# Kernel tuning notes

Measured on AMD Instinct MI355X. Metric: run time of the kernel, lower is better.

Reference implementation:

```python
import jax, jax.numpy as jnp
import numpy as np

DIM = 1024
T = 16384
WINDOW = 32
DIM_HEAD = 64
HEADS = DIM // DIM_HEAD  # 16
EPS = 1e-5


def setup_inputs() -> dict:
    key = jax.random.key(0)
    k1, k2, k3 = jax.random.split(key, 3)
    x = jax.random.normal(k1, (DIM, T), dtype=jnp.float32)
    w_qkv = jax.random.normal(k2, (3 * DIM, DIM), dtype=jnp.float32) / np.float32(np.sqrt(DIM))
    w_out = jax.random.normal(k3, (DIM, DIM), dtype=jnp.float32) / np.float32(np.sqrt(DIM))
    gamma = jnp.ones((DIM,), dtype=jnp.float32)
    beta = jnp.zeros((DIM,), dtype=jnp.float32)
    return {"x": x, "w_qkv": w_qkv, "w_out": w_out, "gamma": gamma, "beta": beta}


def _rotate_half(t):
    # original: split channels into (2, d/2), swap halves with negation
    d = t.shape[-1]
    return jnp.concatenate((-t[..., d // 2:], t[..., :d // 2]), axis=-1)


def reference(x, w_qkv, w_out, gamma, beta):
    C, Tn = x.shape
    xt = x.T  # (T, C)
    # LayerNorm over channel dim (eqx.nn.LayerNorm, eps=1e-5)
    mu = jnp.mean(xt, axis=-1, keepdims=True)
    var = jnp.var(xt, axis=-1, keepdims=True)
    normed = (xt - mu) * jax.lax.rsqrt(var + EPS) * gamma + beta
    # QKV projection (Linear with weight (out,in), no bias)
    qkv = normed @ w_qkv.T  # (T, 3C)
    q, k, v = jnp.split(qkv, 3, axis=-1)
    w = Tn // WINDOW
    def towin(t):  # (w n) (h d) -> h w n d
        return t.reshape(w, WINDOW, HEADS, DIM_HEAD).transpose(2, 0, 1, 3)
    q, k, v = map(towin, (q, k, v))
    # rotary pos emb over window positions (use_xpos=False -> scale == 1)
    inv_freq = 1.0 / (10000.0 ** (jnp.arange(0, DIM_HEAD, 2, dtype=jnp.float32) / DIM_HEAD))
    tpos = jnp.arange(WINDOW, dtype=jnp.float32)
    freqs = jnp.einsum('i,j->ij', tpos, inv_freq)  # (n, d/2)
    freqs = jnp.concatenate((freqs, freqs), axis=-1)  # (n, d)
    cos, sin = jnp.cos(freqs), jnp.sin(freqs)
    q = q * cos + _rotate_half(q) * sin
    k = k * cos + _rotate_half(k) * sin
    # per-head, per-window full (non-causal) attention
    scale = DIM_HEAD ** -0.5
    logits = jnp.einsum('hwnd,hwmd->hwnm', q, k) * scale
    attn = jax.nn.softmax(logits, axis=-1)
    out = jnp.einsum('hwnm,hwmd->hwnd', attn, v)
    out = out.transpose(1, 2, 0, 3).reshape(Tn, C)  # h w n d -> (w n) (h d)
    out = out @ w_out.T
    return out.T + x
```

## Files before the change

### kernel.cpp

```cpp
#include <hip/hip_runtime.h>

#define T_TOK 16384
#define C_DIM 1024

typedef float f32x4 __attribute__((ext_vector_type(4)));
typedef float f32x16 __attribute__((ext_vector_type(16)));
typedef __bf16 bf16x8 __attribute__((ext_vector_type(8)));
typedef unsigned short u16x8 __attribute__((ext_vector_type(8)));
typedef unsigned short u16x4 __attribute__((ext_vector_type(4)));

__device__ __forceinline__ unsigned short f2bf(float f) {
  union { float f; unsigned u; } v; v.f = f;
  unsigned r = v.u + 0x7fffu + ((v.u >> 16) & 1u);
  return (unsigned short)(r >> 16);
}
__device__ __forceinline__ float bf2f(unsigned short h) {
  union { unsigned u; float f; } v; v.u = ((unsigned)h) << 16;
  return v.f;
}
__device__ __forceinline__ unsigned pk2(float a, float b) {
  return (unsigned)f2bf(a) | ((unsigned)f2bf(b) << 16);
}

__global__ __launch_bounds__(256) void cvt_kernel(const float* __restrict__ in,
                                                  unsigned short* __restrict__ out, int n4) {
  int i = blockIdx.x * 256 + threadIdx.x;
  if (i >= n4) return;
  f32x4 v = *(const f32x4*)(in + (size_t)i * 4);
  u16x4 o;
#pragma unroll
  for (int j = 0; j < 4; ++j) o[j] = f2bf(v[j]);
  *(u16x4*)(out + (size_t)i * 4) = o;
}

__global__ __launch_bounds__(256) void rope_tab_kernel(float* __restrict__ tab) {
  int idx = blockIdx.x * 256 + threadIdx.x;
  if (idx >= 1024) return;
  int mm = idx >> 5, d = idx & 31;
  float invf = powf(10000.f, -(float)d * (1.f / 32.f));
  float ang = (float)mm * invf;
  float s, c;
  sincosf(ang, &s, &c);
  tab[idx * 2] = c;
  tab[idx * 2 + 1] = s;
}

__global__ __launch_bounds__(256) void ln_stats_kernel(const float* __restrict__ x,
                                                       float* __restrict__ mu,
                                                       float* __restrict__ rstd) {
  __shared__ float s1[4][64];
  __shared__ float s2[4][64];
  const int tid = threadIdx.x;
  const int lt = tid & 63, cq = tid >> 6;
  const int t = blockIdx.x * 64 + lt;
  float s = 0.f, ss = 0.f;
  const float* p = x + (size_t)cq * 256 * T_TOK + t;
  for (int c = 0; c < 256; ++c) {
    float v = p[(size_t)c * T_TOK];
    s += v; ss += v * v;
  }
  s1[cq][lt] = s; s2[cq][lt] = ss;
  __syncthreads();
  if (tid < 64) {
    float S  = s1[0][tid] + s1[1][tid] + s1[2][tid] + s1[3][tid];
    float SS = s2[0][tid] + s2[1][tid] + s2[2][tid] + s2[3][tid];
    float m = S * (1.f / 1024.f);
    float var = SS * (1.f / 1024.f) - m * m;
    mu[blockIdx.x * 64 + tid] = m;
    rstd[blockIdx.x * 64 + tid] = rsqrtf(var + 1e-5f);
  }
}

__global__ __launch_bounds__(256) void ln_tr_kernel(const float* __restrict__ x,
                                                    const float* __restrict__ mu,
                                                    const float* __restrict__ rstd,
                                                    const float* __restrict__ gamma,
                                                    const float* __restrict__ beta,
                                                    unsigned short* __restrict__ normed) {
  __shared__ float tile[64][65];
  __shared__ float gs[64], bs[64], ms[64], rs[64];
  const int tid = threadIdx.x;
  const int bt = blockIdx.x & 255;
  const int bc = blockIdx.x >> 8;
  const int t0 = bt * 64, c0 = bc * 64;
  if (tid < 64) {
    gs[tid] = gamma[c0 + tid];
    bs[tid] = beta[c0 + tid];
    ms[tid] = mu[t0 + tid];
    rs[tid] = rstd[t0 + tid];
  }
  const int lc = tid >> 4;
  const int lt4 = (tid & 15) * 4;
#pragma unroll
  for (int r = 0; r < 4; ++r) {
    int c = r * 16 + lc;
    f32x4 v = *(const f32x4*)&x[(size_t)(c0 + c) * T_TOK + t0 + lt4];
    tile[c][lt4 + 0] = v[0]; tile[c][lt4 + 1] = v[1];
    tile[c][lt4 + 2] = v[2]; tile[c][lt4 + 3] = v[3];
  }
  __syncthreads();
#pragma unroll
  for (int r = 0; r < 2; ++r) {
    int idx = r * 256 + tid;
    int t = idx >> 3;
    int c8 = (idx & 7) * 8;
    float m = ms[t], rr = rs[t];
    u16x8 o;
#pragma unroll
    for (int j = 0; j < 8; ++j) {
      float v = tile[c8 + j][t];
      v = (v - m) * rr * gs[c8 + j] + bs[c8 + j];
      o[j] = f2bf(v);
    }
    *(u16x8*)&normed[(size_t)(t0 + t) * C_DIM + c0 + c8] = o;
  }
}

#define GLDS(gp, lp) \
  __builtin_amdgcn_global_load_lds((const __attribute__((address_space(1))) void*)(gp), \
                                   (__attribute__((address_space(3))) void*)(lp), 16, 0, 0)

#define BARF() do { __builtin_amdgcn_s_barrier(); asm volatile("" ::: "memory"); } while (0)
#define VMC(n) asm volatile("s_waitcnt vmcnt(" #n ")" ::: "memory")

template <int EPI>
__global__ __launch_bounds__(512, 2) void gemm8p_kernel(const unsigned short* __restrict__ A,
                                                        const unsigned short* __restrict__ B,
                                                        unsigned short* __restrict__ Obf,
                                                        int ldo, int nbn, int K,
                                                        const float* __restrict__ Xadd,
                                                        float* __restrict__ Ofp) {
  __shared__ unsigned short Lds[2][2][2][8192];
  const int tid = threadIdx.x;
  const int w = tid >> 6, lane = tid & 63;
  const int wm = w >> 2, wn = w & 3;

  const int nbm = gridDim.x / nbn;
  const int xcd = blockIdx.x & 7;
  const int ib = blockIdx.x >> 3;
  int mt, nt;
  if ((nbm & 7) == 0) {
    const int mtpx = nbm >> 3;
    mt = xcd * mtpx + (ib % mtpx);
    nt = ib / mtpx;
  } else {
    const int ntpx = nbn >> 3;
    nt = xcd * ntpx + (ib % ntpx);
    mt = ib / ntpx;
  }
  const size_t m0 = (size_t)mt * 256, n0 = (size_t)nt * 256;

  const unsigned short* gA = A + (m0 + (lane >> 3)) * (size_t)K + ((lane & 7) ^ (lane >> 3)) * 8;
  const unsigned short* gB = B + (n0 + (lane >> 3)) * (size_t)K + ((lane & 7) ^ (lane >> 3)) * 8;
  const int wrow = w * 8;

  auto stageA = [&](int b, int h, int kt) {
    const unsigned short* g = gA + (size_t)(h * 128) * K + (size_t)kt * 64;
    GLDS(g + (size_t)wrow * K,        &Lds[0][b][h][wrow * 64]);
    GLDS(g + (size_t)(64 + wrow) * K, &Lds[0][b][h][(64 + wrow) * 64]);
  };
  auto stageB = [&](int b, int h, int kt) {
    const unsigned short* g = gB + (size_t)(h * 128) * K + (size_t)kt * 64;
    GLDS(g + (size_t)wrow * K,        &Lds[1][b][h][wrow * 64]);
    GLDS(g + (size_t)(64 + wrow) * K, &Lds[1][b][h][(64 + wrow) * 64]);
  };

  f32x4 acc[8][4];
#pragma unroll
  for (int i = 0; i < 8; ++i)
#pragma unroll
    for (int j = 0; j < 4; ++j) acc[i][j] = (f32x4){0.f, 0.f, 0.f, 0.f};

  const int KT = K >> 6;
  const int off_r = (lane & 15) * 64;
  const int slot0 = (((lane >> 4) ^ (lane & 7)) * 8);
  const int slot1 = slot0 ^ 32;
  const int boff = (wn & 1) * 4096;

  bf16x8 aLo[4][2], aHi[4][2], bLo[2][2], bHi[2][2];

  stageA(0, 0, 0); stageA(0, 1, 0); stageB(0, 0, 0); stageB(0, 1, 0);
  if (KT > 1) {
    stageB(1, 0, 1); stageB(1, 1, 1); stageA(1, 0, 1); stageA(1, 1, 1);
    VMC(8);
  } else {
    VMC(0);
  }
  BARF();

  int bb = 0;
  for (int t = 0; t < KT; ++t, bb ^= 1) {
    const unsigned short* Ab = &Lds[0][bb][wm][0];
    const unsigned short* Bb = &Lds[1][bb][wn >> 1][boff];

#pragma unroll
    for (int mi = 0; mi < 4; ++mi) {
      aLo[mi][0] = *(const bf16x8*)&Ab[mi * 1024 + off_r + slot0];
      aLo[mi][1] = *(const bf16x8*)&Ab[mi * 1024 + off_r + slot1];
    }
#pragma unroll
    for (int ni = 0; ni < 2; ++ni) {
      bLo[ni][0] = *(const bf16x8*)&Bb[ni * 1024 + off_r + slot0];
      bLo[ni][1] = *(const bf16x8*)&Bb[ni * 1024 + off_r + slot1];
      bHi[ni][0] = *(const bf16x8*)&Bb[(ni + 2) * 1024 + off_r + slot0];
      bHi[ni][1] = *(const bf16x8*)&Bb[(ni + 2) * 1024 + off_r + slot1];
    }

    __builtin_amdgcn_s_setprio(1);
#pragma unroll
    for (int mi = 0; mi < 4; ++mi)
#pragma unroll
      for (int ni = 0; ni < 2; ++ni)
#pragma unroll
        for (int ks = 0; ks < 2; ++ks)
          acc[mi][ni] = __builtin_amdgcn_mfma_f32_16x16x32_bf16(aLo[mi][ks], bLo[ni][ks], acc[mi][ni], 0, 0, 0);
    __builtin_amdgcn_s_setprio(0);

#pragma unroll
    for (int mi = 0; mi < 4; ++mi) {
      aHi[mi][0] = *(const bf16x8*)&Ab[(mi + 4) * 1024 + off_r + slot0];
      aHi[mi][1] = *(const bf16x8*)&Ab[(mi + 4) * 1024 + off_r + slot1];
    }

    __builtin_amdgcn_s_setprio(1);
#pragma unroll
    for (int mi = 0; mi < 4; ++mi)
#pragma unroll
      for (int ni = 0; ni < 2; ++ni)
#pragma unroll
        for (int ks = 0; ks < 2; ++ks)
          acc[mi][ni + 2] = __builtin_amdgcn_mfma_f32_16x16x32_bf16(aLo[mi][ks], bHi[ni][ks], acc[mi][ni + 2], 0, 0, 0);
    __builtin_amdgcn_s_setprio(0);
    BARF();

    if (t + 2 < KT) { stageB(bb, 0, t + 2); stageB(bb, 1, t + 2); }

    __builtin_amdgcn_s_setprio(1);
#pragma unroll
    for (int mi = 0; mi < 4; ++mi)
#pragma unroll
      for (int ni = 0; ni < 2; ++ni)
#pragma unroll
        for (int ks = 0; ks < 2; ++ks)
          acc[mi + 4][ni + 2] = __builtin_amdgcn_mfma_f32_16x16x32_bf16(aHi[mi][ks], bHi[ni][ks], acc[mi + 4][ni + 2], 0, 0, 0);
    __builtin_amdgcn_s_setprio(0);
    BARF();

    if (t + 2 < KT) { stageA(bb, 0, t + 2); stageA(bb, 1, t + 2); }

    __builtin_amdgcn_s_setprio(1);
#pragma unroll
    for (int mi = 0; mi < 4; ++mi)
#pragma unroll
      for (int ni = 0; ni < 2; ++ni)
#pragma unroll
        for (int ks = 0; ks < 2; ++ks)
          acc[mi + 4][ni] = __builtin_amdgcn_mfma_f32_16x16x32_bf16(aHi[mi][ks], bLo[ni][ks], acc[mi + 4][ni], 0, 0, 0);
    __builtin_amdgcn_s_setprio(0);

    if (t + 2 < KT) {
      VMC(8);
    } else {
      VMC(0);
    }
    BARF();
  }

  if (EPI == 0) {
    unsigned short* cw = &Lds[0][0][0][0] + (size_t)w * 8192;
#pragma unroll
    for (int mi = 0; mi < 8; ++mi)
#pragma unroll
      for (int ni = 0; ni < 4; ++ni)
#pragma unroll
        for (int r = 0; r < 4; ++r)
          cw[(mi * 16 + (lane >> 4) * 4 + r) * 64 + ni * 16 + (lane & 15)] = f2bf(acc[mi][ni][r]);
    const size_t gr0 = m0 + wm * 128;
    const size_t gc0 = n0 + wn * 64;
#pragma unroll
    for (int it = 0; it < 16; ++it) {
      int idx = it * 64 + lane;
      int rr = idx >> 3, c8 = (idx & 7) * 8;
      *(u16x8*)&Obf[(gr0 + rr) * (size_t)ldo + gc0 + c8] = *(const u16x8*)&cw[rr * 64 + c8];
    }
  } else {
    const size_t mrow0 = m0 + wm * 128 + (lane >> 4) * 4;
    const size_t ncol0 = n0 + wn * 64 + (lane & 15);
#pragma unroll
    for (int mi = 0; mi < 8; ++mi)
#pragma unroll
      for (int ni = 0; ni < 4; ++ni)
#pragma unroll
        for (int r = 0; r < 4; ++r) {
          size_t o = (mrow0 + mi * 16 + r) * T_TOK + ncol0 + ni * 16;
          Ofp[o] = acc[mi][ni][r] + Xadd[o];
        }
  }
}

__global__ __launch_bounds__(256) void attn_kernel(const unsigned short* __restrict__ qkv,
                                                   const float* __restrict__ ropeT,
                                                   unsigned short* __restrict__ aout) {
  __shared__ unsigned short Vt[4][64][32];
  const int tid = threadIdx.x;
  const int wv = tid >> 6;
  const int lane = tid & 63;
  const int m = lane & 31;
  const int hi = lane >> 5;
  const int gw = blockIdx.x * 4 + wv;
  const int w = gw >> 4, h = gw & 15;
  const size_t rowbase = ((size_t)(w * 32 + m)) * 3072 + (size_t)h * 64;
  const unsigned short* qp = qkv + rowbase;

  u16x8 qv[4], kv[4], vv[4];
#pragma unroll
  for (int s = 0; s < 4; ++s) {
    int off = s * 16 + hi * 8;
    qv[s] = *(const u16x8*)(qp + off);
    kv[s] = *(const u16x8*)(qp + 1024 + off);
    vv[s] = *(const u16x8*)(qp + 2048 + off);
  }

#pragma unroll
  for (int s = 0; s < 4; ++s)
#pragma unroll
    for (int j = 0; j < 8; ++j) {
      int d = s * 16 + hi * 8 + j;
      int slot = (((m >> 3) ^ (d ^ (d >> 2))) & 3) * 8 + (m & 7);
      Vt[wv][d][slot] = vv[s][j];
    }

  f32x4 ct[2][4];
  const float* tp = ropeT + (size_t)(m * 32 + hi * 8) * 2;
#pragma unroll
  for (int kp = 0; kp < 2; ++kp)
#pragma unroll
    for (int q = 0; q < 4; ++q)
      ct[kp][q] = *(const f32x4*)(tp + kp * 32 + q * 4);

  union FU { unsigned u[4]; bf16x8 v; };
  bf16x8 qfr[4], kfr[4];
#pragma unroll
  for (int ks = 0; ks < 4; ++ks) {
    const int kp = ks & 1;
    FU fq, fk;
#pragma unroll
    for (int jp = 0; jp < 4; ++jp) {
      float c0 = ct[kp][jp][0], s0 = ct[kp][jp][1];
      float c1 = ct[kp][jp][2], s1 = ct[kp][jp][3];
      float q0 = bf2f(qv[ks][2 * jp]), q1 = bf2f(qv[ks][2 * jp + 1]);
      float k0 = bf2f(kv[ks][2 * jp]), k1 = bf2f(kv[ks][2 * jp + 1]);
      float rq0, rq1, rk0, rk1;
      if (ks < 2) {
        rq0 = -bf2f(qv[ks + 2][2 * jp]); rq1 = -bf2f(qv[ks + 2][2 * jp + 1]);
        rk0 = -bf2f(kv[ks + 2][2 * jp]); rk1 = -bf2f(kv[ks + 2][2 * jp + 1]);
      } else {
        rq0 = bf2f(qv[ks - 2][2 * jp]); rq1 = bf2f(qv[ks - 2][2 * jp + 1]);
        rk0 = bf2f(kv[ks - 2][2 * jp]); rk1 = bf2f(kv[ks - 2][2 * jp + 1]);
      }
      fq.u[jp] = pk2(q0 * c0 + rq0 * s0, q1 * c1 + rq1 * s1);
      fk.u[jp] = pk2(k0 * c0 + rk0 * s0, k1 * c1 + rk1 * s1);
    }
    qfr[ks] = fq.v; kfr[ks] = fk.v;
  }

  f32x16 accS;
#pragma unroll
  for (int i = 0; i < 16; ++i) accS[i] = 0.f;
#pragma unroll
  for (int ks = 0; ks < 4; ++ks)
    accS = __builtin_amdgcn_mfma_f32_32x32x16_bf16(kfr[ks], qfr[ks], accS, 0, 0, 0);

  float p[16];
  float mx = -1e30f;
#pragma unroll
  for (int r = 0; r < 16; ++r) { p[r] = accS[r] * 0.125f; mx = fmaxf(mx, p[r]); }
  mx = fmaxf(mx, __shfl_xor(mx, 32, 64));
  float sum = 0.f;
#pragma unroll
  for (int r = 0; r < 16; ++r) { p[r] = __expf(p[r] - mx); sum += p[r]; }
  sum += __shfl_xor(sum, 32, 64);
  const float inv = 1.f / sum;
#pragma unroll
  for (int r = 0; r < 16; ++r) p[r] *= inv;

  bf16x8 pfr[2];
  {
    FU f0, f1;
    unsigned a0 = hi ? pk2(p[0], p[1]) : pk2(p[4], p[5]);
    unsigned a1 = hi ? pk2(p[2], p[3]) : pk2(p[6], p[7]);
    unsigned b0 = (unsigned)__shfl_xor((int)a0, 32, 64);
    unsigned b1 = (unsigned)__shfl_xor((int)a1, 32, 64);
    if (hi) { f0.u[0] = b0; f0.u[1] = b1; f0.u[2] = pk2(p[4], p[5]); f0.u[3] = pk2(p[6], p[7]); }
    else    { f0.u[0] = pk2(p[0], p[1]); f0.u[1] = pk2(p[2], p[3]); f0.u[2] = b0; f0.u[3] = b1; }
    unsigned a2 = hi ? pk2(p[8], p[9])   : pk2(p[12], p[13]);
    unsigned a3 = hi ? pk2(p[10], p[11]) : pk2(p[14], p[15]);
    unsigned b2 = (unsigned)__shfl_xor((int)a2, 32, 64);
    unsigned b3 = (unsigned)__shfl_xor((int)a3, 32, 64);
    if (hi) { f1.u[0] = b2; f1.u[1] = b3; f1.u[2] = pk2(p[12], p[13]); f1.u[3] = pk2(p[14], p[15]); }
    else    { f1.u[0] = pk2(p[8], p[9]); f1.u[1] = pk2(p[10], p[11]); f1.u[2] = b2; f1.u[3] = b3; }
    pfr[0] = f0.v; pfr[1] = f1.v;
  }

  f32x16 accO[2];
#pragma unroll
  for (int i = 0; i < 16; ++i) { accO[0][i] = 0.f; accO[1][i] = 0.f; }
  const int dl = lane & 31;
#pragma unroll
  for (int dh = 0; dh < 2; ++dh) {
    int d = dh * 32 + dl;
    int sx = (d ^ (d >> 2)) & 3;
#pragma unroll
    for (int ks = 0; ks < 2; ++ks) {
      bf16x8 vf = *(const bf16x8*)&Vt[wv][d][(((2 * ks + hi) ^ sx) & 3) * 8];
      accO[dh] = __builtin_amdgcn_mfma_f32_32x32x16_bf16(pfr[ks], vf, accO[dh], 0, 0, 0);
    }
  }

#pragma unroll
  for (int r = 0; r < 16; ++r) {
    int n = (r & 3) + 8 * (r >> 2) + 4 * hi;
    size_t o = (size_t)(w * 32 + n) * 1024 + h * 64 + dl;
    aout[o] = f2bf(accO[0][r]);
    aout[o + 32] = f2bf(accO[1][r]);
  }
}

extern "C" void kernel_launch(void* const* d_in, const int* in_sizes, int n_in,
                              void* d_out, int out_size, void* d_ws, size_t ws_size,
                              hipStream_t stream) {
  const float* x     = (const float*)d_in[0];
  const float* w_qkv = (const float*)d_in[1];
  const float* w_out = (const float*)d_in[2];
  const float* gamma = (const float*)d_in[3];
  const float* beta  = (const float*)d_in[4];

  char* ws = (char*)d_ws;
  unsigned short* wqkv_bf = (unsigned short*)(ws);
  unsigned short* wout_bf = (unsigned short*)(ws + 6291456);
  float* mu    = (float*)(ws + 8388608);
  float* rstd  = (float*)(ws + 8454144);
  float* ropeT = (float*)(ws + 8519680);
  unsigned short* normed = (unsigned short*)(ws + 8527872);
  unsigned short* qkv    = (unsigned short*)(ws + 42082304);
  unsigned short* aout   = normed;

  cvt_kernel<<<3072, 256, 0, stream>>>(w_qkv, wqkv_bf, 3072 * 1024 / 4);
  cvt_kernel<<<1024, 256, 0, stream>>>(w_out, wout_bf, 1024 * 1024 / 4);
  rope_tab_kernel<<<4, 256, 0, stream>>>(ropeT);
  ln_stats_kernel<<<256, 256, 0, stream>>>(x, mu, rstd);
  ln_tr_kernel<<<4096, 256, 0, stream>>>(x, mu, rstd, gamma, beta, normed);
  gemm8p_kernel<0><<<768, 512, 0, stream>>>(normed, wqkv_bf, qkv, 3072, 12, 1024,
                                            nullptr, nullptr);
  attn_kernel<<<2048, 256, 0, stream>>>(qkv, ropeT, aout);
  gemm8p_kernel<1><<<256, 512, 0, stream>>>(wout_bf, aout, nullptr, 0, 64, 1024,
                                            x, (float*)d_out);
}
```

Baseline: 211.3 us.

## Fuse QKV projection GEMM with windowed attention in one kernel

After: 205.8 us. 2.6% less time.

```diff
diff --git a/kernel.cpp b/kernel.cpp
--- a/kernel.cpp
+++ b/kernel.cpp
@@ -123,6 +123,226 @@
 #define BARF() do { __builtin_amdgcn_s_barrier(); asm volatile("" ::: "memory"); } while (0)
 #define VMC(n) asm volatile("s_waitcnt vmcnt(" #n ")" ::: "memory")
 
+__global__ __launch_bounds__(512, 2) void qkvattn_kernel(const unsigned short* __restrict__ A,
+                                                         const unsigned short* __restrict__ Bq,
+                                                         const float* __restrict__ ropeT,
+                                                         unsigned short* __restrict__ aout) {
+  __shared__ unsigned short arena[57344];
+  unsigned short* LA = arena;
+  unsigned short* LB = arena + 32768;
+  unsigned short* QKl = arena;
+  unsigned short* Vtl = arena + 34816;
+
+  const int tid = threadIdx.x;
+  const int w = tid >> 6, lane = tid & 63;
+  const int wm = w >> 1, wn = w & 1;
+  const int K = 1024, KT = 16;
+
+  const int xcd = blockIdx.x & 7;
+  const int ib = blockIdx.x >> 3;
+  const int tt = xcd * 8 + (ib & 7);
+  const int h = ib >> 3;
+  const size_t m0 = (size_t)tt * 256;
+
+  const int preslot = ((lane & 7) ^ (lane >> 3)) * 8;
+  const unsigned short* gA = A + (m0 + w * 8 + (lane >> 3)) * (size_t)K + preslot;
+  const unsigned short* gB0 = Bq + ((size_t)(0 + h * 64 + w * 8 + (lane >> 3))) * K + preslot;
+  const unsigned short* gB1 = Bq + ((size_t)(1024 + h * 64 + w * 8 + (lane >> 3))) * K + preslot;
+  const unsigned short* gB2 = Bq + ((size_t)(2048 + h * 64 + w * 8 + (lane >> 3))) * K + preslot;
+
+  auto stage7 = [&](int b, int kt) {
+    const size_t k0 = (size_t)kt * 64;
+    GLDS(gA + k0,                      LA + b * 16384 + (w * 8) * 64);
+    GLDS(gA + (size_t)64 * K + k0,     LA + b * 16384 + (64 + w * 8) * 64);
+    GLDS(gA + (size_t)128 * K + k0,    LA + b * 16384 + (128 + w * 8) * 64);
+    GLDS(gA + (size_t)192 * K + k0,    LA + b * 16384 + (192 + w * 8) * 64);
+    GLDS(gB0 + k0,                     LB + b * 12288 + (w * 8) * 64);
+    GLDS(gB1 + k0,                     LB + b * 12288 + (64 + w * 8) * 64);
+    GLDS(gB2 + k0,                     LB + b * 12288 + (128 + w * 8) * 64);
+  };
+
+  f32x4 acc[4][6];
+#pragma unroll
+  for (int i = 0; i < 4; ++i)
+#pragma unroll
+    for (int j = 0; j < 6; ++j) acc[i][j] = (f32x4){0.f, 0.f, 0.f, 0.f};
+
+  const int off_r = (lane & 15) * 64;
+  const int slot0 = (((lane >> 4) ^ (lane & 7)) * 8);
+  const int slot1 = slot0 ^ 32;
+
+  stage7(0, 0);
+  stage7(1, 1);
+  VMC(7);
+  BARF();
+
+  int bb = 0;
+  for (int t = 0; t < KT; ++t, bb ^= 1) {
+    const unsigned short* Ab = LA + bb * 16384 + (wm * 64) * 64;
+    const unsigned short* Bb = LB + bb * 12288 + (wn * 96) * 64;
+
+    bf16x8 aF[4][2], bF[6][2];
+#pragma unroll
+    for (int mi = 0; mi < 4; ++mi) {
+      aF[mi][0] = *(const bf16x8*)&Ab[mi * 1024 + off_r + slot0];
+      aF[mi][1] = *(const bf16x8*)&Ab[mi * 1024 + off_r + slot1];
+    }
+#pragma unroll
+    for (int ni = 0; ni < 6; ++ni) {
+      bF[ni][0] = *(const bf16x8*)&Bb[ni * 1024 + off_r + slot0];
+      bF[ni][1] = *(const bf16x8*)&Bb[ni * 1024 + off_r + slot1];
+    }
+
+    __builtin_amdgcn_s_setprio(1);
+#pragma unroll
+    for (int mi = 0; mi < 4; ++mi)
+#pragma unroll
+      for (int ni = 0; ni < 6; ++ni)
+#pragma unroll
+        for (int ks = 0; ks < 2; ++ks)
+          acc[mi][ni] = __builtin_amdgcn_mfma_f32_16x16x32_bf16(aF[mi][ks], bF[ni][ks], acc[mi][ni], 0, 0, 0);
+    __builtin_amdgcn_s_setprio(0);
+    BARF();
+
+    if (t + 2 < KT) {
+      stage7(bb, t + 2);
+      VMC(7);
+    } else {
+      VMC(0);
+    }
+    BARF();
+  }
+
+  __syncthreads();
+#pragma unroll
+  for (int mi = 0; mi < 4; ++mi)
+#pragma unroll
+    for (int ni = 0; ni < 6; ++ni) {
+      const int j = wn * 96 + ni * 16 + (lane & 15);
+#pragma unroll
+      for (int r = 0; r < 4; ++r) {
+        int tok = wm * 64 + mi * 16 + (lane >> 4) * 4 + r;
+        unsigned short bv = f2bf(acc[mi][ni][r]);
+        if (wn == 0 || ni < 2) {
+          QKl[tok * 136 + j] = bv;
+        } else {
+          int d = j - 128;
+          int mm = tok & 31, win = tok >> 5;
+          Vtl[(win * 64 + d) * 32 + ((((mm >> 3) ^ (d ^ (d >> 2))) & 3) * 8 + (mm & 7))] = bv;
+        }
+      }
+    }
+  __syncthreads();
+
+  {
+    const int m = lane & 31, hi = lane >> 5;
+    const unsigned short* qp = QKl + (size_t)(w * 32 + m) * 136;
+    u16x8 qv[4], kv[4];
+#pragma unroll
+    for (int s = 0; s < 4; ++s) {
+      int off = s * 16 + hi * 8;
+      qv[s] = *(const u16x8*)(qp + off);
+      kv[s] = *(const u16x8*)(qp + 64 + off);
+    }
+
+    f32x4 ct[2][4];
+    const float* tp = ropeT + (size_t)(m * 32 + hi * 8) * 2;
+#pragma unroll
+    for (int kp = 0; kp < 2; ++kp)
+#pragma unroll
+      for (int q = 0; q < 4; ++q)
+        ct[kp][q] = *(const f32x4*)(tp + kp * 32 + q * 4);
+
+    union FU { unsigned u[4]; bf16x8 v; };
+    bf16x8 qfr[4], kfr[4];
+#pragma unroll
+    for (int ks = 0; ks < 4; ++ks) {
+      const int kp = ks & 1;
+      FU fq, fk;
+#pragma unroll
+      for (int jp = 0; jp < 4; ++jp) {
+        float c0 = ct[kp][jp][0], s0 = ct[kp][jp][1];
+        float c1 = ct[kp][jp][2], s1 = ct[kp][jp][3];
+        float q0 = bf2f(qv[ks][2 * jp]), q1 = bf2f(qv[ks][2 * jp + 1]);
+        float k0 = bf2f(kv[ks][2 * jp]), k1 = bf2f(kv[ks][2 * jp + 1]);
+        float rq0, rq1, rk0, rk1;
+        if (ks < 2) {
+          rq0 = -bf2f(qv[ks + 2][2 * jp]); rq1 = -bf2f(qv[ks + 2][2 * jp + 1]);
+          rk0 = -bf2f(kv[ks + 2][2 * jp]); rk1 = -bf2f(kv[ks + 2][2 * jp + 1]);
+        } else {
+          rq0 = bf2f(qv[ks - 2][2 * jp]); rq1 = bf2f(qv[ks - 2][2 * jp + 1]);
+          rk0 = bf2f(kv[ks - 2][2 * jp]); rk1 = bf2f(kv[ks - 2][2 * jp + 1]);
+        }
+        fq.u[jp] = pk2(q0 * c0 + rq0 * s0, q1 * c1 + rq1 * s1);
+        fk.u[jp] = pk2(k0 * c0 + rk0 * s0, k1 * c1 + rk1 * s1);
+      }
+      qfr[ks] = fq.v; kfr[ks] = fk.v;
+    }
+
+    f32x16 accS;
+#pragma unroll
+    for (int i = 0; i < 16; ++i) accS[i] = 0.f;
+#pragma unroll
+    for (int ks = 0; ks < 4; ++ks)
+      accS = __builtin_amdgcn_mfma_f32_32x32x16_bf16(kfr[ks], qfr[ks], accS, 0, 0, 0);
+
+    float p[16];
+    float mx = -1e30f;
+#pragma unroll
+    for (int r = 0; r < 16; ++r) { p[r] = accS[r] * 0.125f; mx = fmaxf(mx, p[r]); }
+    mx = fmaxf(mx, __shfl_xor(mx, 32, 64));
+    float sum = 0.f;
+#pragma unroll
+    for (int r = 0; r < 16; ++r) { p[r] = __expf(p[r] - mx); sum += p[r]; }
+    sum += __shfl_xor(sum, 32, 64);
+    const float inv = 1.f / sum;
+#pragma unroll
+    for (int r = 0; r < 16; ++r) p[r] *= inv;
+
+    bf16x8 pfr[2];
+    {
+      FU f0, f1;
+      unsigned a0 = hi ? pk2(p[0], p[1]) : pk2(p[4], p[5]);
+      unsigned a1 = hi ? pk2(p[2], p[3]) : pk2(p[6], p[7]);
+      unsigned b0 = (unsigned)__shfl_xor((int)a0, 32, 64);
+      unsigned b1 = (unsigned)__shfl_xor((int)a1, 32, 64);
+      if (hi) { f0.u[0] = b0; f0.u[1] = b1; f0.u[2] = pk2(p[4], p[5]); f0.u[3] = pk2(p[6], p[7]); }
+      else    { f0.u[0] = pk2(p[0], p[1]); f0.u[1] = pk2(p[2], p[3]); f0.u[2] = b0; f0.u[3] = b1; }
+      unsigned a2 = hi ? pk2(p[8], p[9])   : pk2(p[12], p[13]);
+      unsigned a3 = hi ? pk2(p[10], p[11]) : pk2(p[14], p[15]);
+      unsigned b2 = (unsigned)__shfl_xor((int)a2, 32, 64);
+      unsigned b3 = (unsigned)__shfl_xor((int)a3, 32, 64);
+      if (hi) { f1.u[0] = b2; f1.u[1] = b3; f1.u[2] = pk2(p[12], p[13]); f1.u[3] = pk2(p[14], p[15]); }
+      else    { f1.u[0] = pk2(p[8], p[9]); f1.u[1] = pk2(p[10], p[11]); f1.u[2] = b2; f1.u[3] = b3; }
+      pfr[0] = f0.v; pfr[1] = f1.v;
+    }
+
+    f32x16 accO[2];
+#pragma unroll
+    for (int i = 0; i < 16; ++i) { accO[0][i] = 0.f; accO[1][i] = 0.f; }
+    const int dl = lane & 31;
+#pragma unroll
+    for (int dh = 0; dh < 2; ++dh) {
+      int d = dh * 32 + dl;
+      int sx = (d ^ (d >> 2)) & 3;
+#pragma unroll
+      for (int ks = 0; ks < 2; ++ks) {
+        bf16x8 vf = *(const bf16x8*)&Vtl[(w * 64 + d) * 32 + (((2 * ks + hi) ^ sx) & 3) * 8];
+        accO[dh] = __builtin_amdgcn_mfma_f32_32x32x16_bf16(pfr[ks], vf, accO[dh], 0, 0, 0);
+      }
+    }
+
+    const int W = tt * 8 + w;
+#pragma unroll
+    for (int r = 0; r < 16; ++r) {
+      int n = (r & 3) + 8 * (r >> 2) + 4 * hi;
+      size_t o = (size_t)(W * 32 + n) * 1024 + h * 64 + dl;
+      aout[o] = f2bf(accO[0][r]);
+      aout[o + 32] = f2bf(accO[1][r]);
+    }
+  }
+}
+
 template <int EPI>
 __global__ __launch_bounds__(512, 2) void gemm8p_kernel(const unsigned short* __restrict__ A,
                                                         const unsigned short* __restrict__ B,
@@ -298,134 +518,6 @@
   }
 }
 
-__global__ __launch_bounds__(256) void attn_kernel(const unsigned short* __restrict__ qkv,
-                                                   const float* __restrict__ ropeT,
-                                                   unsigned short* __restrict__ aout) {
-  __shared__ unsigned short Vt[4][64][32];
-  const int tid = threadIdx.x;
-  const int wv = tid >> 6;
-  const int lane = tid & 63;
-  const int m = lane & 31;
-  const int hi = lane >> 5;
-  const int gw = blockIdx.x * 4 + wv;
-  const int w = gw >> 4, h = gw & 15;
-  const size_t rowbase = ((size_t)(w * 32 + m)) * 3072 + (size_t)h * 64;
-  const unsigned short* qp = qkv + rowbase;
-
-  u16x8 qv[4], kv[4], vv[4];
-#pragma unroll
-  for (int s = 0; s < 4; ++s) {
-    int off = s * 16 + hi * 8;
-    qv[s] = *(const u16x8*)(qp + off);
-    kv[s] = *(const u16x8*)(qp + 1024 + off);
-    vv[s] = *(const u16x8*)(qp + 2048 + off);
-  }
-
-#pragma unroll
-  for (int s = 0; s < 4; ++s)
-#pragma unroll
-    for (int j = 0; j < 8; ++j) {
-      int d = s * 16 + hi * 8 + j;
-      int slot = (((m >> 3) ^ (d ^ (d >> 2))) & 3) * 8 + (m & 7);
-      Vt[wv][d][slot] = vv[s][j];
-    }
-
-  f32x4 ct[2][4];
-  const float* tp = ropeT + (size_t)(m * 32 + hi * 8) * 2;
-#pragma unroll
-  for (int kp = 0; kp < 2; ++kp)
-#pragma unroll
-    for (int q = 0; q < 4; ++q)
-      ct[kp][q] = *(const f32x4*)(tp + kp * 32 + q * 4);
-
-  union FU { unsigned u[4]; bf16x8 v; };
-  bf16x8 qfr[4], kfr[4];
-#pragma unroll
-  for (int ks = 0; ks < 4; ++ks) {
-    const int kp = ks & 1;
-    FU fq, fk;
-#pragma unroll
-    for (int jp = 0; jp < 4; ++jp) {
-      float c0 = ct[kp][jp][0], s0 = ct[kp][jp][1];
-      float c1 = ct[kp][jp][2], s1 = ct[kp][jp][3];
-      float q0 = bf2f(qv[ks][2 * jp]), q1 = bf2f(qv[ks][2 * jp + 1]);
-      float k0 = bf2f(kv[ks][2 * jp]), k1 = bf2f(kv[ks][2 * jp + 1]);
-      float rq0, rq1, rk0, rk1;
-      if (ks < 2) {
-        rq0 = -bf2f(qv[ks + 2][2 * jp]); rq1 = -bf2f(qv[ks + 2][2 * jp + 1]);
-        rk0 = -bf2f(kv[ks + 2][2 * jp]); rk1 = -bf2f(kv[ks + 2][2 * jp + 1]);
-      } else {
-        rq0 = bf2f(qv[ks - 2][2 * jp]); rq1 = bf2f(qv[ks - 2][2 * jp + 1]);
-        rk0 = bf2f(kv[ks - 2][2 * jp]); rk1 = bf2f(kv[ks - 2][2 * jp + 1]);
-      }
-      fq.u[jp] = pk2(q0 * c0 + rq0 * s0, q1 * c1 + rq1 * s1);
-      fk.u[jp] = pk2(k0 * c0 + rk0 * s0, k1 * c1 + rk1 * s1);
-    }
-    qfr[ks] = fq.v; kfr[ks] = fk.v;
-  }
-
-  f32x16 accS;
-#pragma unroll
-  for (int i = 0; i < 16; ++i) accS[i] = 0.f;
-#pragma unroll
-  for (int ks = 0; ks < 4; ++ks)
-    accS = __builtin_amdgcn_mfma_f32_32x32x16_bf16(kfr[ks], qfr[ks], accS, 0, 0, 0);
-
-  float p[16];
-  float mx = -1e30f;
-#pragma unroll
-  for (int r = 0; r < 16; ++r) { p[r] = accS[r] * 0.125f; mx = fmaxf(mx, p[r]); }
-  mx = fmaxf(mx, __shfl_xor(mx, 32, 64));
-  float sum = 0.f;
-#pragma unroll
-  for (int r = 0; r < 16; ++r) { p[r] = __expf(p[r] - mx); sum += p[r]; }
-  sum += __shfl_xor(sum, 32, 64);
-  const float inv = 1.f / sum;
-#pragma unroll
-  for (int r = 0; r < 16; ++r) p[r] *= inv;
-
-  bf16x8 pfr[2];
-  {
-    FU f0, f1;
-    unsigned a0 = hi ? pk2(p[0], p[1]) : pk2(p[4], p[5]);
-    unsigned a1 = hi ? pk2(p[2], p[3]) : pk2(p[6], p[7]);
-    unsigned b0 = (unsigned)__shfl_xor((int)a0, 32, 64);
-    unsigned b1 = (unsigned)__shfl_xor((int)a1, 32, 64);
-    if (hi) { f0.u[0] = b0; f0.u[1] = b1; f0.u[2] = pk2(p[4], p[5]); f0.u[3] = pk2(p[6], p[7]); }
-    else    { f0.u[0] = pk2(p[0], p[1]); f0.u[1] = pk2(p[2], p[3]); f0.u[2] = b0; f0.u[3] = b1; }
-    unsigned a2 = hi ? pk2(p[8], p[9])   : pk2(p[12], p[13]);
-    unsigned a3 = hi ? pk2(p[10], p[11]) : pk2(p[14], p[15]);
-    unsigned b2 = (unsigned)__shfl_xor((int)a2, 32, 64);
-    unsigned b3 = (unsigned)__shfl_xor((int)a3, 32, 64);
-    if (hi) { f1.u[0] = b2; f1.u[1] = b3; f1.u[2] = pk2(p[12], p[13]); f1.u[3] = pk2(p[14], p[15]); }
-    else    { f1.u[0] = pk2(p[8], p[9]); f1.u[1] = pk2(p[10], p[11]); f1.u[2] = b2; f1.u[3] = b3; }
-    pfr[0] = f0.v; pfr[1] = f1.v;
-  }
-
-  f32x16 accO[2];
-#pragma unroll
-  for (int i = 0; i < 16; ++i) { accO[0][i] = 0.f; accO[1][i] = 0.f; }
-  const int dl = lane & 31;
-#pragma unroll
-  for (int dh = 0; dh < 2; ++dh) {
-    int d = dh * 32 + dl;
-    int sx = (d ^ (d >> 2)) & 3;
-#pragma unroll
-    for (int ks = 0; ks < 2; ++ks) {
-      bf16x8 vf = *(const bf16x8*)&Vt[wv][d][(((2 * ks + hi) ^ sx) & 3) * 8];
-      accO[dh] = __builtin_amdgcn_mfma_f32_32x32x16_bf16(pfr[ks], vf, accO[dh], 0, 0, 0);
-    }
-  }
-
-#pragma unroll
-  for (int r = 0; r < 16; ++r) {
-    int n = (r & 3) + 8 * (r >> 2) + 4 * hi;
-    size_t o = (size_t)(w * 32 + n) * 1024 + h * 64 + dl;
-    aout[o] = f2bf(accO[0][r]);
-    aout[o + 32] = f2bf(accO[1][r]);
-  }
-}
-
 extern "C" void kernel_launch(void* const* d_in, const int* in_sizes, int n_in,
                               void* d_out, int out_size, void* d_ws, size_t ws_size,
                               hipStream_t stream) {
@@ -442,17 +534,14 @@
   float* rstd  = (float*)(ws + 8454144);
   float* ropeT = (float*)(ws + 8519680);
   unsigned short* normed = (unsigned short*)(ws + 8527872);
-  unsigned short* qkv    = (unsigned short*)(ws + 42082304);
-  unsigned short* aout   = normed;
+  unsigned short* aout   = (unsigned short*)(ws + 42082304);
 
   cvt_kernel<<<3072, 256, 0, stream>>>(w_qkv, wqkv_bf, 3072 * 1024 / 4);
   cvt_kernel<<<1024, 256, 0, stream>>>(w_out, wout_bf, 1024 * 1024 / 4);
   rope_tab_kernel<<<4, 256, 0, stream>>>(ropeT);
   ln_stats_kernel<<<256, 256, 0, stream>>>(x, mu, rstd);
   ln_tr_kernel<<<4096, 256, 0, stream>>>(x, mu, rstd, gamma, beta, normed);
-  gemm8p_kernel<0><<<768, 512, 0, stream>>>(normed, wqkv_bf, qkv, 3072, 12, 1024,
-                                            nullptr, nullptr);
-  attn_kernel<<<2048, 256, 0, stream>>>(qkv, ropeT, aout);
+  qkvattn_kernel<<<1024, 512, 0, stream>>>(normed, wqkv_bf, ropeT, aout);
   gemm8p_kernel<1><<<256, 512, 0, stream>>>(wout_bf, aout, nullptr, 0, 64, 1024,
                                             x, (float*)d_out);
 }
```
